# Optimization experiments

Measured on AMD Instinct MI355X. Metric: run time of the kernel, lower is better.

## Reference

```python
import jax, jax.numpy as jnp
import numpy as np

NBINS = 10001  # hardcoded in the torch module (10000*sigmoid in [0,10000])


def setup_inputs() -> dict:
    key = jax.random.key(0)
    k1, k2 = jax.random.split(key)
    N = 33554432  # 2**25 samples
    preds = jax.random.normal(k1, (N,), dtype=jnp.float32)
    targets = jax.random.randint(k2, (N,), 0, 2).astype(jnp.float32)
    return {"preds": preds, "targets": targets}


def reference(preds, targets):
    # y_pred = int(10000 * sigmoid(preds)); truncation == floor since value >= 0
    y_pred = (10000.0 * jax.nn.sigmoid(preds)).reshape(-1).astype(jnp.int32)
    y_true = targets.reshape(-1)
    is_pos = (y_true >= 0.5).astype(preds.dtype)
    # scatter-add histogram split by label (single pass, atomic-add style)
    tpi = jnp.zeros((NBINS,), dtype=preds.dtype).at[y_pred].add(is_pos)
    fpi = jnp.zeros((NBINS,), dtype=preds.dtype).at[y_pred].add(1.0 - is_pos)
    # KS statistic: max |CDF_pos - CDF_neg|
    tp_cum = jnp.cumsum(tpi)
    fp_cum = jnp.cumsum(fpi)
    tp_curve = tp_cum / tp_cum[-1]
    fp_curve = fp_cum / fp_cum[-1]
    return jnp.max(jnp.abs(tp_curve - fp_curve))
```

## Files before the change

kernel.cpp:

```cpp
#include <hip/hip_runtime.h>

#define NBINS 10001
#define ROWP  10016
#define HIST_BLOCKS 768
#define HIST_THREADS 512

typedef unsigned int u32;
typedef unsigned long long u64;
typedef float f4 __attribute__((ext_vector_type(4)));

__device__ __forceinline__ int ks_bin(float x) {
    float e = __expf(-x);
    float s = __builtin_amdgcn_rcpf(1.0f + e);
    int b = (int)(10000.0f * s);
    b = b < 0 ? 0 : b;
    return b > 10000 ? 10000 : b;
}

__device__ __forceinline__ void ks_acc4(u32* lh, f4 p, f4 t) {
#pragma unroll
    for (int k = 0; k < 4; ++k) {
        int b = ks_bin(p[k]);
        u32 add = (t[k] >= 0.5f) ? 0x10000u : 1u;
        atomicAdd(&lh[b], add);
    }
}

__global__ __launch_bounds__(HIST_THREADS) void ks_hist(
        const float* __restrict__ preds, const float* __restrict__ tgts,
        u64* __restrict__ ghist, u32* __restrict__ partials,
        int use_partials, int n) {
    __shared__ u32 lh[NBINS];
    for (int i = threadIdx.x; i < NBINS; i += HIST_THREADS) lh[i] = 0u;
    __syncthreads();

    const int n4 = n >> 2;
    const f4* p4 = (const f4*)preds;
    const f4* t4 = (const f4*)tgts;
    const int tid = blockIdx.x * HIST_THREADS + threadIdx.x;
    const int stride = gridDim.x * HIST_THREADS;

    int i = tid;
    for (; i + 3 * stride < n4; i += 4 * stride) {
        f4 p0 = p4[i];
        f4 t0 = t4[i];
        f4 p1 = p4[i + stride];
        f4 t1 = t4[i + stride];
        f4 p2 = p4[i + 2 * stride];
        f4 t2 = t4[i + 2 * stride];
        f4 p3 = p4[i + 3 * stride];
        f4 t3 = t4[i + 3 * stride];
        ks_acc4(lh, p0, t0);
        ks_acc4(lh, p1, t1);
        ks_acc4(lh, p2, t2);
        ks_acc4(lh, p3, t3);
    }
    for (; i < n4; i += stride) {
        f4 p = p4[i];
        f4 t = t4[i];
        ks_acc4(lh, p, t);
    }

    if (blockIdx.x == 0) {
        int base = n4 << 2;
        int rem = n - base;
        if ((int)threadIdx.x < rem) {
            int j = base + threadIdx.x;
            int b = ks_bin(preds[j]);
            u32 add = (tgts[j] >= 0.5f) ? 0x10000u : 1u;
            atomicAdd(&lh[b], add);
        }
    }
    __syncthreads();

    if (use_partials) {
        u32* mypart = partials + (size_t)blockIdx.x * ROWP;
        for (int b = threadIdx.x; b < NBINS; b += HIST_THREADS)
            mypart[b] = lh[b];
    } else {
        for (int b = threadIdx.x; b < NBINS; b += HIST_THREADS) {
            u32 v = lh[b];
            if (v) {
                u64 a = ((u64)(v >> 16) << 32) | (u64)(v & 0xFFFFu);
                atomicAdd(&ghist[b], a);
            }
        }
    }
}

__global__ __launch_bounds__(256) void ks_reduce(const u32* __restrict__ partials,
                                                 u64* __restrict__ ghist) {
    int bin = blockIdx.x * 256 + threadIdx.x;
    if (bin >= NBINS) return;
    const u32* base = partials + bin;
    u32 tp = 0, fp = 0;
#pragma unroll 8
    for (int k = 0; k < HIST_BLOCKS; ++k) {
        u32 v = base[(size_t)k * ROWP];
        tp += v >> 16;
        fp += v & 0xFFFFu;
    }
    ghist[bin] = ((u64)tp << 32) | (u64)fp;
}

__global__ __launch_bounds__(1024) void ks_scan(const u64* __restrict__ ghist,
                                                float* __restrict__ out) {
    __shared__ long long stp[1024];
    __shared__ long long sfp[1024];
    __shared__ double smx[1024];

    const int t = threadIdx.x;
    const int CH = 10;
    const int lo = t * CH;

    u64 loc[CH];
    long long tps = 0, fps = 0;
#pragma unroll
    for (int k = 0; k < CH; ++k) {
        int i = lo + k;
        u64 v = (i < NBINS) ? ghist[i] : 0ull;
        loc[k] = v;
        tps += (long long)(v >> 32);
        fps += (long long)(v & 0xFFFFFFFFull);
    }
    stp[t] = tps;
    sfp[t] = fps;
    __syncthreads();

    for (int off = 1; off < 1024; off <<= 1) {
        long long a = stp[t], b = sfp[t];
        long long c = 0, d = 0;
        if (t >= off) { c = stp[t - off]; d = sfp[t - off]; }
        __syncthreads();
        stp[t] = a + c;
        sfp[t] = b + d;
        __syncthreads();
    }

    const long long TP = stp[1023];
    const long long FP = sfp[1023];
    const long long etp = stp[t] - tps;
    const long long efp = sfp[t] - fps;

    const double invTP = 1.0 / (double)(TP > 0 ? TP : 1);
    const double invFP = 1.0 / (double)(FP > 0 ? FP : 1);

    double m = 0.0;
    long long tc = etp, fc = efp;
#pragma unroll
    for (int k = 0; k < CH; ++k) {
        u64 v = loc[k];
        tc += (long long)(v >> 32);
        fc += (long long)(v & 0xFFFFFFFFull);
        double d = fabs((double)tc * invTP - (double)fc * invFP);
        m = (d > m) ? d : m;
    }

    smx[t] = m;
    __syncthreads();
    for (int off = 512; off > 0; off >>= 1) {
        if (t < off) smx[t] = smx[t] > smx[t + off] ? smx[t] : smx[t + off];
        __syncthreads();
    }
    if (t == 0) out[0] = (float)smx[0];
}

extern "C" void kernel_launch(void* const* d_in, const int* in_sizes, int n_in,
                              void* d_out, int out_size, void* d_ws, size_t ws_size,
                              hipStream_t stream) {
    const float* preds = (const float*)d_in[0];
    const float* tgts  = (const float*)d_in[1];
    const int n = in_sizes[0];

    const size_t part_off = 131072;
    const size_t need = part_off + (size_t)HIST_BLOCKS * ROWP * sizeof(u32);
    u64* ghist = (u64*)d_ws;
    u32* partials = (u32*)((char*)d_ws + part_off);
    const int use_partials = (ws_size >= need) ? 1 : 0;

    if (!use_partials)
        hipMemsetAsync(d_ws, 0, NBINS * sizeof(u64), stream);

    ks_hist<<<HIST_BLOCKS, HIST_THREADS, 0, stream>>>(preds, tgts, ghist,
                                                      partials, use_partials, n);
    if (use_partials) {
        ks_reduce<<<(NBINS + 255) / 256, 256, 0, stream>>>(partials, ghist);
    }
    ks_scan<<<1, 1024, 0, stream>>>(ghist, (float*)d_out);
}
```

Measured before the change: 83.06 us.

## Fuse partial reduction and scan with last-block ticket, widen reduce grid

Replaces the separate reduce and single-block scan kernels with one kernel that splits the partial-histogram reduction across row chunks, atomically accumulates into the global histogram, and lets the last finishing block perform the CDF scan and max. This removes one kernel launch and spreads the reduce over more blocks. Target loads become nontemporal and a redundant clamp is dropped. In exchange it adds a memset on every call, global atomics, and a threadfence/ticket protocol whose correctness depends on memory ordering.

```diff
diff --git a/kernel.cpp b/kernel.cpp
--- a/kernel.cpp
+++ b/kernel.cpp
@@ -4,6 +4,9 @@
 #define ROWP  10016
 #define HIST_BLOCKS 768
 #define HIST_THREADS 512
+#define PCHUNK 128
+#define RCOLS ((NBINS + 255) / 256)
+#define RGRID (RCOLS * (HIST_BLOCKS / PCHUNK))
 
 typedef unsigned int u32;
 typedef unsigned long long u64;
@@ -13,7 +16,6 @@
     float e = __expf(-x);
     float s = __builtin_amdgcn_rcpf(1.0f + e);
     int b = (int)(10000.0f * s);
-    b = b < 0 ? 0 : b;
     return b > 10000 ? 10000 : b;
 }
 
@@ -43,13 +45,13 @@
     int i = tid;
     for (; i + 3 * stride < n4; i += 4 * stride) {
         f4 p0 = p4[i];
-        f4 t0 = t4[i];
+        f4 t0 = __builtin_nontemporal_load(t4 + i);
         f4 p1 = p4[i + stride];
-        f4 t1 = t4[i + stride];
+        f4 t1 = __builtin_nontemporal_load(t4 + i + stride);
         f4 p2 = p4[i + 2 * stride];
-        f4 t2 = t4[i + 2 * stride];
+        f4 t2 = __builtin_nontemporal_load(t4 + i + 2 * stride);
         f4 p3 = p4[i + 3 * stride];
-        f4 t3 = t4[i + 3 * stride];
+        f4 t3 = __builtin_nontemporal_load(t4 + i + 3 * stride);
         ks_acc4(lh, p0, t0);
         ks_acc4(lh, p1, t1);
         ks_acc4(lh, p2, t2);
@@ -57,7 +59,7 @@
     }
     for (; i < n4; i += stride) {
         f4 p = p4[i];
-        f4 t = t4[i];
+        f4 t = __builtin_nontemporal_load(t4 + i);
         ks_acc4(lh, p, t);
     }
 
@@ -88,19 +90,89 @@
     }
 }
 
-__global__ __launch_bounds__(256) void ks_reduce(const u32* __restrict__ partials,
-                                                 u64* __restrict__ ghist) {
-    int bin = blockIdx.x * 256 + threadIdx.x;
-    if (bin >= NBINS) return;
-    const u32* base = partials + bin;
-    u32 tp = 0, fp = 0;
-#pragma unroll 8
-    for (int k = 0; k < HIST_BLOCKS; ++k) {
-        u32 v = base[(size_t)k * ROWP];
-        tp += v >> 16;
-        fp += v & 0xFFFFu;
-    }
-    ghist[bin] = ((u64)tp << 32) | (u64)fp;
+__global__ __launch_bounds__(256) void ks_reduce_scan(
+        const u32* __restrict__ partials, u64* __restrict__ ghist,
+        u32* __restrict__ counter, float* __restrict__ out) {
+    __shared__ long long stp[256];
+    __shared__ long long sfp[256];
+    __shared__ double smx[256];
+    __shared__ u32 s_ticket;
+
+    const int t = threadIdx.x;
+    const int col = blockIdx.x % RCOLS;
+    const int row = blockIdx.x / RCOLS;
+    const int bin = col * 256 + t;
+
+    if (bin < NBINS) {
+        const u32* base = partials + (size_t)row * PCHUNK * ROWP + bin;
+        u32 tp = 0, fp = 0;
+#pragma unroll 4
+        for (int k = 0; k < PCHUNK; ++k) {
+            u32 v = base[(size_t)k * ROWP];
+            tp += v >> 16;
+            fp += v & 0xFFFFu;
+        }
+        if (tp | fp) atomicAdd(&ghist[bin], ((u64)tp << 32) | (u64)fp);
+    }
+
+    __threadfence();
+    if (t == 0) s_ticket = atomicAdd(counter, 1u);
+    __syncthreads();
+    if (s_ticket != RGRID - 1) return;
+
+    const int CH = 40;
+    const int lo = t * CH;
+    long long tps = 0, fps = 0;
+    for (int k = 0; k < CH; ++k) {
+        int i = lo + k;
+        if (i < NBINS) {
+            u64 v = __hip_atomic_load(&ghist[i], __ATOMIC_RELAXED,
+                                      __HIP_MEMORY_SCOPE_AGENT);
+            tps += (long long)(v >> 32);
+            fps += (long long)(v & 0xFFFFFFFFull);
+        }
+    }
+    stp[t] = tps;
+    sfp[t] = fps;
+    __syncthreads();
+
+    for (int off = 1; off < 256; off <<= 1) {
+        long long a = stp[t], b = sfp[t];
+        long long c = 0, d = 0;
+        if (t >= off) { c = stp[t - off]; d = sfp[t - off]; }
+        __syncthreads();
+        stp[t] = a + c;
+        sfp[t] = b + d;
+        __syncthreads();
+    }
+
+    const long long TP = stp[255];
+    const long long FP = sfp[255];
+    const double invTP = 1.0 / (double)(TP > 0 ? TP : 1);
+    const double invFP = 1.0 / (double)(FP > 0 ? FP : 1);
+
+    long long tc = stp[t] - tps;
+    long long fc = sfp[t] - fps;
+    double m = 0.0;
+    for (int k = 0; k < CH; ++k) {
+        int i = lo + k;
+        if (i < NBINS) {
+            u64 v = __hip_atomic_load(&ghist[i], __ATOMIC_RELAXED,
+                                      __HIP_MEMORY_SCOPE_AGENT);
+            tc += (long long)(v >> 32);
+            fc += (long long)(v & 0xFFFFFFFFull);
+            double d = fabs((double)tc * invTP - (double)fc * invFP);
+            m = (d > m) ? d : m;
+        }
+    }
+
+    smx[t] = m;
+    __syncthreads();
+    for (int off = 128; off > 0; off >>= 1) {
+        if (t < off) smx[t] = smx[t] > smx[t + off] ? smx[t] : smx[t + off];
+        __syncthreads();
+    }
+    if (t == 0) out[0] = (float)smx[0];
 }
 
 __global__ __launch_bounds__(1024) void ks_scan(const u64* __restrict__ ghist,
@@ -141,7 +213,6 @@
     const long long FP = sfp[1023];
     const long long etp = stp[t] - tps;
     const long long efp = sfp[t] - fps;
-
     const double invTP = 1.0 / (double)(TP > 0 ? TP : 1);
     const double invFP = 1.0 / (double)(FP > 0 ? FP : 1);
 
@@ -172,19 +243,22 @@
     const float* tgts  = (const float*)d_in[1];
     const int n = in_sizes[0];
 
+    const size_t ctr_off = 80384;
     const size_t part_off = 131072;
     const size_t need = part_off + (size_t)HIST_BLOCKS * ROWP * sizeof(u32);
     u64* ghist = (u64*)d_ws;
+    u32* counter = (u32*)((char*)d_ws + ctr_off);
     u32* partials = (u32*)((char*)d_ws + part_off);
     const int use_partials = (ws_size >= need) ? 1 : 0;
 
-    if (!use_partials)
-        hipMemsetAsync(d_ws, 0, NBINS * sizeof(u64), stream);
+    hipMemsetAsync(d_ws, 0, ctr_off + sizeof(u32), stream);
 
     ks_hist<<<HIST_BLOCKS, HIST_THREADS, 0, stream>>>(preds, tgts, ghist,
                                                       partials, use_partials, n);
     if (use_partials) {
-        ks_reduce<<<(NBINS + 255) / 256, 256, 0, stream>>>(partials, ghist);
-    }
-    ks_scan<<<1, 1024, 0, stream>>>(ghist, (float*)d_out);
-}
+        ks_reduce_scan<<<RGRID, 256, 0, stream>>>(partials, ghist, counter,
+                                                  (float*)d_out);
+    } else {
+        ks_scan<<<1, 1024, 0, stream>>>(ghist, (float*)d_out);
+    }
+}
```

New measurement: 99.14 us. +19.4%, slower.
